# Optimization experiments

Measured on AMD Instinct MI355X. Metric: run time of the kernel, lower is better.

Reference implementation:

```python
import jax, jax.numpy as jnp
import numpy as np

EPS = 1e-8
N_IN = 200000   # x.shape[0]
N_OUT = 100000  # pool_map.shape[0]
NNZ = 800000
C = 256
HIDDEN = C // 2


def setup_inputs() -> dict:
    key = jax.random.key(0)
    ks = jax.random.split(key, 8)
    x = jax.random.normal(ks[0], (N_IN, C), dtype=jnp.float32)
    vals = jax.random.uniform(ks[1], (NNZ,), dtype=jnp.float32)
    rows = jnp.sort(jax.random.randint(ks[2], (NNZ,), 0, N_OUT, dtype=jnp.int64))
    cols = jax.random.randint(ks[3], (NNZ,), 0, N_IN, dtype=jnp.int64)
    # gate MLP params (Linear(C, C//2) -> GELU -> Linear(C//2, 1))
    W1 = jax.random.normal(ks[4], (C, HIDDEN), dtype=jnp.float32) * (1.0 / np.sqrt(C))
    b1 = jnp.zeros((HIDDEN,), dtype=jnp.float32)
    W2 = jax.random.normal(ks[5], (HIDDEN, 1), dtype=jnp.float32) * (1.0 / np.sqrt(HIDDEN))
    b2 = jnp.zeros((1,), dtype=jnp.float32)
    return {"x": x, "vals": vals, "rows": rows, "cols": cols,
            "W1": W1, "b1": b1, "W2": W2, "b2": b2}


def reference(x, vals, rows, cols, W1, b1, W2, b2):
    # gate MLP: Linear -> exact GELU -> Linear -> sigmoid, per input element
    h = jax.nn.gelu(x @ W1 + b1, approximate=False)          # [N_IN, HIDDEN]
    gates = jax.nn.sigmoid((h @ W2 + b2)[:, 0])              # [N_IN]
    # gate the sparse pool-map values by their source column's gate
    gv = vals * gates[cols]                                   # [NNZ]
    # mass = gated_pool @ ones ; pooled = (gated_pool @ x) / clamp(mass)
    # (segment_sum also sums duplicate (row,col) entries == coalesce)
    mass = jax.ops.segment_sum(gv, rows, num_segments=N_OUT)  # [N_OUT]
    num = jax.ops.segment_sum(gv[:, None] * x[cols], rows, num_segments=N_OUT)  # [N_OUT, C]
    return num / jnp.maximum(mass, EPS)[:, None]
```

## Files before the change

### kernel.cpp

```cpp
#include <hip/hip_runtime.h>
#include <hip/hip_bf16.h>
#include <math.h>

typedef float f32x4 __attribute__((ext_vector_type(4)));
typedef short bf16x8 __attribute__((ext_vector_type(8)));

#define C_DIM 256
#define HID 128

__device__ __forceinline__ unsigned short f2bf(float f) {
  unsigned u = __builtin_bit_cast(unsigned, f);
  u = (u + 0x7fffu + ((u >> 16) & 1u)) >> 16;
  return (unsigned short)u;
}

__global__ __launch_bounds__(256) void prep_w_kernel(const float* __restrict__ W1,
                                                     unsigned short* __restrict__ wbuf) {
  int i = blockIdx.x * 256 + threadIdx.x;
  int jj = i & 7;
  int l  = (i >> 3) & 63;
  int nt = (i >> 9) & 7;
  int kc = i >> 12;
  int k   = kc * 32 + (l >> 4) * 8 + jj;
  int col = nt * 16 + (l & 15);
  wbuf[i] = f2bf(W1[k * HID + col]);
}

__global__ __launch_bounds__(256) void offs_kernel(const int* __restrict__ rows,
                                                   int* __restrict__ offs,
                                                   int nnz, int n_out) {
  int e = blockIdx.x * 256 + threadIdx.x;
  if (e >= nnz) return;
  int r  = rows[e];
  int rp = (e == 0) ? -1 : rows[e - 1];
  for (int rr = rp + 1; rr <= r; ++rr) offs[rr] = e;
  if (e == nnz - 1) {
    for (int rr = r + 1; rr <= n_out; ++rr) offs[rr] = nnz;
  }
}

__global__ __launch_bounds__(256) void gates_kernel(
    const float* __restrict__ x, const unsigned short* __restrict__ wbuf,
    const float* __restrict__ b1, const float* __restrict__ W2,
    const float* __restrict__ b2, float* __restrict__ gates, int n_in) {
  __shared__ unsigned short ldsw[32768];
  {
    const f32x4* src = (const f32x4*)wbuf;
    f32x4* dst = (f32x4*)ldsw;
#pragma unroll
    for (int i = 0; i < 16; ++i) dst[threadIdx.x + i * 256] = src[threadIdx.x + i * 256];
  }
  __syncthreads();

  const int lane = threadIdx.x & 63;
  const int wid  = threadIdx.x >> 6;
  const int rowbase = blockIdx.x * 128 + wid * 32;
  const int kgrp = lane >> 4;
  const int colbase = lane & 15;

  int ar0 = rowbase + colbase;        if (ar0 >= n_in) ar0 = n_in - 1;
  int ar1 = rowbase + 16 + colbase;   if (ar1 >= n_in) ar1 = n_in - 1;

  f32x4 acc[2][8];
#pragma unroll
  for (int g = 0; g < 2; ++g)
#pragma unroll
    for (int nt = 0; nt < 8; ++nt) acc[g][nt] = (f32x4){0.f, 0.f, 0.f, 0.f};

  const float* xr0 = x + (size_t)ar0 * C_DIM + kgrp * 8;
  const float* xr1 = x + (size_t)ar1 * C_DIM + kgrp * 8;

#pragma unroll
  for (int kc = 0; kc < 8; ++kc) {
    f32x4 a0l = *(const f32x4*)(xr0 + kc * 32);
    f32x4 a0h = *(const f32x4*)(xr0 + kc * 32 + 4);
    f32x4 a1l = *(const f32x4*)(xr1 + kc * 32);
    f32x4 a1h = *(const f32x4*)(xr1 + kc * 32 + 4);
    bf16x8 af0, af1;
#pragma unroll
    for (int j = 0; j < 4; ++j) {
      af0[j] = (short)f2bf(a0l[j]); af0[4 + j] = (short)f2bf(a0h[j]);
      af1[j] = (short)f2bf(a1l[j]); af1[4 + j] = (short)f2bf(a1h[j]);
    }
#pragma unroll
    for (int nt = 0; nt < 8; ++nt) {
      bf16x8 wf = *(const bf16x8*)(ldsw + ((kc * 8 + nt) * 64 + lane) * 8);
      acc[0][nt] = __builtin_amdgcn_mfma_f32_16x16x32_bf16(af0, wf, acc[0][nt], 0, 0, 0);
      acc[1][nt] = __builtin_amdgcn_mfma_f32_16x16x32_bf16(af1, wf, acc[1][nt], 0, 0, 0);
    }
  }

  float bb[8], w2[8];
#pragma unroll
  for (int nt = 0; nt < 8; ++nt) {
    int hid = nt * 16 + colbase;
    bb[nt] = b1[hid];
    w2[nt] = W2[hid];
  }
  const float bb2 = b2[0];
  const float kA = 0.7978845608028654f;
  const float kB = 0.044715f;

#pragma unroll
  for (int g = 0; g < 2; ++g) {
    float s[4] = {0.f, 0.f, 0.f, 0.f};
#pragma unroll
    for (int nt = 0; nt < 8; ++nt) {
#pragma unroll
      for (int r = 0; r < 4; ++r) {
        float v = acc[g][nt][r] + bb[nt];
        float z = kA * (v + kB * v * v * v);
        float a = __expf(-2.0f * fabsf(z));
        float t = (1.0f - a) / (1.0f + a);
        t = (z < 0.0f) ? -t : t;
        float gelu = 0.5f * v * (1.0f + t);
        s[r] += gelu * w2[nt];
      }
    }
#pragma unroll
    for (int m = 1; m < 16; m <<= 1) {
#pragma unroll
      for (int r = 0; r < 4; ++r) s[r] += __shfl_xor(s[r], m, 64);
    }
    if (colbase == 0) {
#pragma unroll
      for (int r = 0; r < 4; ++r) {
        int row = rowbase + g * 16 + kgrp * 4 + r;
        if (row < n_in) {
          float zz = s[r] + bb2;
          gates[row] = 1.0f / (1.0f + __expf(-zz));
        }
      }
    }
  }
}

__global__ __launch_bounds__(256) void pool_kernel(
    const float* __restrict__ x, const float* __restrict__ vals,
    const int* __restrict__ cols, const float* __restrict__ gates,
    const int* __restrict__ offs, float* __restrict__ out, int n_out) {
  const int lane = threadIdx.x & 63;
  const int wid  = threadIdx.x >> 6;
  const int r = blockIdx.x * 4 + wid;
  if (r >= n_out) return;

  const int start = offs[r];
  const int cnt   = offs[r + 1] - start;

  f32x4 acc = (f32x4){0.f, 0.f, 0.f, 0.f};
  float mass = 0.f;

  for (int base = 0; base < cnt; base += 64) {
    const int rem = cnt - base;
    int myc = 0;
    float mygv = 0.f;
    if (lane < rem) {
      int e = start + base + lane;
      myc = cols[e];
      mygv = vals[e] * gates[myc];
    }
    const int m4 = (rem < 64) ? ((rem + 3) & ~3) : 64;
    for (int j = 0; j < m4; j += 4) {
#pragma unroll
      for (int jj = 0; jj < 4; ++jj) {
        const int   c  = __shfl(myc, j + jj, 64);
        const float gv = __shfl(mygv, j + jj, 64);
        const f32x4 xv = *(const f32x4*)(x + (size_t)c * C_DIM + lane * 4);
        acc += gv * xv;
        mass += gv;
      }
    }
  }

  const float inv = 1.0f / fmaxf(mass, 1e-8f);
  f32x4 o = acc * inv;
  __builtin_nontemporal_store(o, (f32x4*)(out + (size_t)r * C_DIM + lane * 4));
}

extern "C" void kernel_launch(void* const* d_in, const int* in_sizes, int n_in_arrs,
                              void* d_out, int out_size, void* d_ws, size_t ws_size,
                              hipStream_t stream) {
  const float* x    = (const float*)d_in[0];
  const float* vals = (const float*)d_in[1];
  const int*   rows = (const int*)d_in[2];
  const int*   cols = (const int*)d_in[3];
  const float* W1   = (const float*)d_in[4];
  const float* b1   = (const float*)d_in[5];
  const float* W2   = (const float*)d_in[6];
  const float* b2   = (const float*)d_in[7];
  float* out = (float*)d_out;

  const int n_in  = in_sizes[0] / C_DIM;
  const int nnz   = in_sizes[1];
  const int n_out = out_size / C_DIM;

  unsigned short* wbuf = (unsigned short*)d_ws;
  float* gates = (float*)((char*)d_ws + (64 << 10));
  int*   offs  = (int*)((char*)d_ws + (64 << 10) + 4 * (size_t)n_in);

  prep_w_kernel<<<128, 256, 0, stream>>>(W1, wbuf);
  offs_kernel<<<(nnz + 255) / 256, 256, 0, stream>>>(rows, offs, nnz, n_out);
  gates_kernel<<<(n_in + 127) / 128, 256, 0, stream>>>(x, wbuf, b1, W2, b2, gates, n_in);
  pool_kernel<<<(n_out + 3) / 4, 256, 0, stream>>>(x, vals, cols, gates, offs, out, n_out);
}
```

Baseline: 477.7 us.

## Gather bf16 copy of x in pooling and precompute gated edge values

The gate kernel now also writes a bf16 copy of x while converting it for MFMA. The pooling kernel gathers rows from this half-size copy instead of fp32 x, which halves the random-gather traffic. Gated values vals*gates[cols] are computed once in a merged edge/offsets kernel that runs after the gates kernel, so the pooling loop no longer does the dependent gates lookup. The cost is an extra write of about 100 MB of bf16 data and reduced precision in the pooled sums. A workspace-size check falls back to an fp32 path when there is not enough space.

```diff
diff --git a/kernel.cpp b/kernel.cpp
--- a/kernel.cpp
+++ b/kernel.cpp
@@ -4,6 +4,7 @@
 
 typedef float f32x4 __attribute__((ext_vector_type(4)));
 typedef short bf16x8 __attribute__((ext_vector_type(8)));
+typedef unsigned short u16x4 __attribute__((ext_vector_type(4)));
 
 #define C_DIM 256
 #define HID 128
@@ -12,6 +13,9 @@
   unsigned u = __builtin_bit_cast(unsigned, f);
   u = (u + 0x7fffu + ((u >> 16) & 1u)) >> 16;
   return (unsigned short)u;
+}
+__device__ __forceinline__ float bf2f(unsigned short h) {
+  return __builtin_bit_cast(float, (unsigned)h << 16);
 }
 
 __global__ __launch_bounds__(256) void prep_w_kernel(const float* __restrict__ W1,
@@ -26,9 +30,10 @@
   wbuf[i] = f2bf(W1[k * HID + col]);
 }
 
-__global__ __launch_bounds__(256) void offs_kernel(const int* __restrict__ rows,
-                                                   int* __restrict__ offs,
-                                                   int nnz, int n_out) {
+__global__ __launch_bounds__(256) void edge_kernel(
+    const int* __restrict__ rows, const int* __restrict__ cols,
+    const float* __restrict__ vals, const float* __restrict__ gates,
+    float* __restrict__ gv, int* __restrict__ offs, int nnz, int n_out) {
   int e = blockIdx.x * 256 + threadIdx.x;
   if (e >= nnz) return;
   int r  = rows[e];
@@ -37,12 +42,15 @@
   if (e == nnz - 1) {
     for (int rr = r + 1; rr <= n_out; ++rr) offs[rr] = nnz;
   }
-}
-
+  gv[e] = vals[e] * gates[cols[e]];
+}
+
+template <bool WRITE_XBF>
 __global__ __launch_bounds__(256) void gates_kernel(
     const float* __restrict__ x, const unsigned short* __restrict__ wbuf,
     const float* __restrict__ b1, const float* __restrict__ W2,
-    const float* __restrict__ b2, float* __restrict__ gates, int n_in) {
+    const float* __restrict__ b2, float* __restrict__ gates,
+    unsigned short* __restrict__ xbf, int n_in) {
   __shared__ unsigned short ldsw[32768];
   {
     const f32x4* src = (const f32x4*)wbuf;
@@ -81,6 +89,10 @@
     for (int j = 0; j < 4; ++j) {
       af0[j] = (short)f2bf(a0l[j]); af0[4 + j] = (short)f2bf(a0h[j]);
       af1[j] = (short)f2bf(a1l[j]); af1[4 + j] = (short)f2bf(a1h[j]);
+    }
+    if (WRITE_XBF) {
+      *(bf16x8*)(xbf + (size_t)ar0 * C_DIM + kc * 32 + kgrp * 8) = af0;
+      *(bf16x8*)(xbf + (size_t)ar1 * C_DIM + kc * 32 + kgrp * 8) = af1;
     }
 #pragma unroll
     for (int nt = 0; nt < 8; ++nt) {
@@ -135,10 +147,10 @@
   }
 }
 
-__global__ __launch_bounds__(256) void pool_kernel(
-    const float* __restrict__ x, const float* __restrict__ vals,
-    const int* __restrict__ cols, const float* __restrict__ gates,
-    const int* __restrict__ offs, float* __restrict__ out, int n_out) {
+__global__ __launch_bounds__(256) void pool_bf16_kernel(
+    const unsigned short* __restrict__ xbf, const float* __restrict__ gv,
+    const int* __restrict__ cols, const int* __restrict__ offs,
+    float* __restrict__ out, int n_out) {
   const int lane = threadIdx.x & 63;
   const int wid  = threadIdx.x >> 6;
   const int r = blockIdx.x * 4 + wid;
@@ -157,17 +169,62 @@
     if (lane < rem) {
       int e = start + base + lane;
       myc = cols[e];
-      mygv = vals[e] * gates[myc];
+      mygv = gv[e];
     }
     const int m4 = (rem < 64) ? ((rem + 3) & ~3) : 64;
     for (int j = 0; j < m4; j += 4) {
 #pragma unroll
       for (int jj = 0; jj < 4; ++jj) {
-        const int   c  = __shfl(myc, j + jj, 64);
-        const float gv = __shfl(mygv, j + jj, 64);
+        const int   c = __shfl(myc, j + jj, 64);
+        const float g = __shfl(mygv, j + jj, 64);
+        const u16x4 xv = *(const u16x4*)(xbf + (size_t)c * C_DIM + lane * 4);
+        acc[0] += g * bf2f(xv[0]);
+        acc[1] += g * bf2f(xv[1]);
+        acc[2] += g * bf2f(xv[2]);
+        acc[3] += g * bf2f(xv[3]);
+        mass += g;
+      }
+    }
+  }
+
+  const float inv = 1.0f / fmaxf(mass, 1e-8f);
+  f32x4 o = acc * inv;
+  __builtin_nontemporal_store(o, (f32x4*)(out + (size_t)r * C_DIM + lane * 4));
+}
+
+__global__ __launch_bounds__(256) void pool_f32_kernel(
+    const float* __restrict__ x, const float* __restrict__ gv,
+    const int* __restrict__ cols, const int* __restrict__ offs,
+    float* __restrict__ out, int n_out) {
+  const int lane = threadIdx.x & 63;
+  const int wid  = threadIdx.x >> 6;
+  const int r = blockIdx.x * 4 + wid;
+  if (r >= n_out) return;
+
+  const int start = offs[r];
+  const int cnt   = offs[r + 1] - start;
+
+  f32x4 acc = (f32x4){0.f, 0.f, 0.f, 0.f};
+  float mass = 0.f;
+
+  for (int base = 0; base < cnt; base += 64) {
+    const int rem = cnt - base;
+    int myc = 0;
+    float mygv = 0.f;
+    if (lane < rem) {
+      int e = start + base + lane;
+      myc = cols[e];
+      mygv = gv[e];
+    }
+    const int m4 = (rem < 64) ? ((rem + 3) & ~3) : 64;
+    for (int j = 0; j < m4; j += 4) {
+#pragma unroll
+      for (int jj = 0; jj < 4; ++jj) {
+        const int   c = __shfl(myc, j + jj, 64);
+        const float g = __shfl(mygv, j + jj, 64);
         const f32x4 xv = *(const f32x4*)(x + (size_t)c * C_DIM + lane * 4);
-        acc += gv * xv;
-        mass += gv;
+        acc += g * xv;
+        mass += g;
       }
     }
   }
@@ -194,12 +251,26 @@
   const int nnz   = in_sizes[1];
   const int n_out = out_size / C_DIM;
 
-  unsigned short* wbuf = (unsigned short*)d_ws;
-  float* gates = (float*)((char*)d_ws + (64 << 10));
-  int*   offs  = (int*)((char*)d_ws + (64 << 10) + 4 * (size_t)n_in);
+  size_t off = 0;
+  unsigned short* wbuf = (unsigned short*)((char*)d_ws + off); off += 64 << 10;
+  float* gates = (float*)((char*)d_ws + off);                  off += 4 * (size_t)n_in;
+  int*   offs  = (int*)((char*)d_ws + off);                    off += 4 * ((size_t)n_out + 1);
+  float* gv    = (float*)((char*)d_ws + off);                  off += 4 * (size_t)nnz;
+  off = (off + 255) & ~(size_t)255;
+  unsigned short* xbf = (unsigned short*)((char*)d_ws + off);
+  const size_t need_xbf = off + 2 * (size_t)n_in * C_DIM;
+  const bool use_bf16 = (ws_size >= need_xbf);
 
   prep_w_kernel<<<128, 256, 0, stream>>>(W1, wbuf);
-  offs_kernel<<<(nnz + 255) / 256, 256, 0, stream>>>(rows, offs, nnz, n_out);
-  gates_kernel<<<(n_in + 127) / 128, 256, 0, stream>>>(x, wbuf, b1, W2, b2, gates, n_in);
-  pool_kernel<<<(n_out + 3) / 4, 256, 0, stream>>>(x, vals, cols, gates, offs, out, n_out);
-}
+  if (use_bf16) {
+    gates_kernel<true><<<(n_in + 127) / 128, 256, 0, stream>>>(x, wbuf, b1, W2, b2, gates, xbf, n_in);
+  } else {
+    gates_kernel<false><<<(n_in + 127) / 128, 256, 0, stream>>>(x, wbuf, b1, W2, b2, gates, xbf, n_in);
+  }
+  edge_kernel<<<(nnz + 255) / 256, 256, 0, stream>>>(rows, cols, vals, gates, gv, offs, nnz, n_out);
+  if (use_bf16) {
+    pool_bf16_kernel<<<(n_out + 3) / 4, 256, 0, stream>>>(xbf, gv, cols, offs, out, n_out);
+  } else {
+    pool_f32_kernel<<<(n_out + 3) / 4, 256, 0, stream>>>(x, gv, cols, offs, out, n_out);
+  }
+}
```

New measurement: 423.7 us. 1.13x faster.
